# Performance work log

Measured on AMD Instinct MI355X. Metric: run time of the kernel, lower is better.

The kernel has to match this reference:

```python
import jax, jax.numpy as jnp
import numpy as np

B, S, E, D = 4, 2048, 1024, 64  # batch, seq, embed_size, low-rank d; dv = E

def setup_inputs() -> dict:
    key = jax.random.key(0)
    ks = jax.random.split(key, 10)
    sc_e = 1.0 / np.sqrt(E)
    sc_d = 1.0 / np.sqrt(D)
    return {
        "x": jax.random.normal(ks[0], (B, S, E), jnp.float32),
        "y": jax.random.normal(ks[1], (B, S, E), jnp.float32),
        "Wq": jax.random.uniform(ks[2], (D, E), jnp.float32, -sc_e, sc_e),
        "bq": jax.random.uniform(ks[3], (D,), jnp.float32, -sc_e, sc_e),
        "Wk": jax.random.uniform(ks[4], (D, E), jnp.float32, -sc_e, sc_e),
        "bk": jax.random.uniform(ks[5], (D,), jnp.float32, -sc_e, sc_e),
        "WvR": jax.random.uniform(ks[6], (D, E), jnp.float32, -sc_e, sc_e),
        "bvR": jax.random.uniform(ks[7], (D,), jnp.float32, -sc_e, sc_e),
        "WvL": jax.random.uniform(ks[8], (E, D), jnp.float32, -sc_d, sc_d),
        "bvL": jax.random.uniform(ks[9], (E,), jnp.float32, -sc_d, sc_d),
    }

def reference(x, y, Wq, bq, Wk, bk, WvR, bvR, WvL, bvL):
    d = Wq.shape[0]
    Q = jnp.einsum('bse,de->bsd', x, Wq) + bq            # [B,S,D]
    K = jnp.einsum('bse,de->bsd', y, Wk) + bk            # [B,S,D]
    scores = jnp.einsum('bqd,bkd->bqk', Q, K) / jnp.sqrt(jnp.float32(d))
    # NOTE: original softmaxes over dim=1, i.e. the QUERY axis (faithful quirk)
    attn = jax.nn.softmax(scores, axis=1)                # [B,Sq,Sk]
    V = jnp.einsum('bsd,vd->bsv', jnp.einsum('bse,de->bsd', y, WvR) + bvR, WvL) + bvL  # [B,S,E]
    return jnp.einsum('bqk,bkv->bqv', attn, V)           # [B,S,E]
```

## Files before the change

### kernel.cpp

```cpp
#include <hip/hip_runtime.h>
#include <hip/hip_bf16.h>

#define DEV static __device__ __forceinline__
#define AS1 __attribute__((address_space(1)))
#define AS3 __attribute__((address_space(3)))

typedef __attribute__((ext_vector_type(8))) short bf16x8;
typedef __attribute__((ext_vector_type(4))) short bf16x4;
typedef __attribute__((ext_vector_type(4))) float f32x4;

constexpr int NB = 4;
constexpr int SS = 2048;
constexpr int EE = 1024;
constexpr int DD = 64;
constexpr int MTOT = NB * SS;

#define QSCALE (0.125f * 1.44269504088896340736f)

DEV short f2bf(float f) {
    union { float f; unsigned u; } v; v.f = f;
    unsigned u = v.u;
    u += 0x7FFFu + ((u >> 16) & 1u);
    return (short)(u >> 16);
}
DEV float bf2f(short h) {
    union { unsigned u; float f; } v; v.u = ((unsigned)(unsigned short)h) << 16;
    return v.f;
}
DEV unsigned pk2(float a, float b) {
    unsigned r;
    asm("v_cvt_pk_bf16_f32 %0, %1, %2" : "=v"(r) : "v"(a), "v"(b));
    return r;
}

DEV f32x4 mfma16(bf16x8 a, bf16x8 b, f32x4 c) {
    return __builtin_amdgcn_mfma_f32_16x16x32_bf16(a, b, c, 0, 0, 0);
}

DEV float redmax16(float v) {
    v = fmaxf(v, __shfl_xor(v, 1)); v = fmaxf(v, __shfl_xor(v, 2));
    v = fmaxf(v, __shfl_xor(v, 4)); v = fmaxf(v, __shfl_xor(v, 8));
    return v;
}
DEV float redsum16(float v) {
    v += __shfl_xor(v, 1); v += __shfl_xor(v, 2);
    v += __shfl_xor(v, 4); v += __shfl_xor(v, 8);
    return v;
}


__global__ __launch_bounds__(256) void k_prep(
    const float* __restrict__ Wq, const float* __restrict__ Wk,
    const float* __restrict__ Wv, const float* __restrict__ WvL,
    const float* __restrict__ bvL,
    short* __restrict__ Wqb, short* __restrict__ Wkb, short* __restrict__ Wvb,
    short* __restrict__ Wcat2)
{
    int g = blockIdx.x * 256 + threadIdx.x;
    if (g < 24576) {
        int mat = g >> 13;
        int c = g & 8191;
        int lane = c & 63;
        int fn = (c >> 6) & 3;
        int it = (c >> 8) & 7;
        int kq4 = c >> 11;
        int r = lane & 15, half = lane >> 4;
        int row = fn * 16 + r;
        int col = kq4 * 256 + it * 32 + half * 4;
        const float* W = (mat == 0) ? Wq : ((mat == 1) ? Wk : Wv);
        short* O = (mat == 0) ? Wqb : ((mat == 1) ? Wkb : Wvb);
        float s = (mat == 0) ? QSCALE : 1.0f;
        const float* Wp = W + (size_t)row * EE + col;
        float4 u = *(const float4*)(Wp);
        float4 v = *(const float4*)(Wp + 16);
        bf16x8 o;
        unsigned* ou = (unsigned*)&o;
        ou[0] = pk2(u.x * s, u.y * s);
        ou[1] = pk2(u.z * s, u.w * s);
        ou[2] = pk2(v.x * s, v.y * s);
        ou[3] = pk2(v.z * s, v.w * s);
        *(bf16x8*)(O + (size_t)c * 8) = o;
    } else {
        int i2 = g - 24576;
        int lane = i2 & 63;
        int ks = (i2 >> 6) % 5;
        int vt = i2 / 320;
        int r = lane & 15, h = lane >> 4;
        int v = vt * 16 + r;
        bf16x8 o;
        #pragma unroll
        for (int j = 0; j < 8; ++j) {
            int c = ks * 16 + (h & 1) * 8 + j;
            float val = (c < 64) ? WvL[(size_t)v * DD + c] : ((c == 64) ? bvL[v] : 0.f);
            o[j] = f2bf(val);
        }
        *(bf16x8*)(Wcat2 + ((size_t)(vt * 5 + ks) * 64 + lane) * 8) = o;
    }
}

__global__ __launch_bounds__(256, 4) void k_proj(
    const float* __restrict__ x, const float* __restrict__ y,
    const short* __restrict__ Wqb, const short* __restrict__ Wkb,
    const short* __restrict__ Wvb,
    const float* __restrict__ bq, const float* __restrict__ bk,
    const float* __restrict__ bv,
    short* __restrict__ Qf, short* __restrict__ Kf, short* __restrict__ VF)
{
    const int tid = threadIdx.x, wave = tid >> 6, lane = tid & 63;
    const int r = lane & 15, half = lane >> 4;
    const int rb = blockIdx.x * 16;
    const bool isQ = (blockIdx.y == 0);
    const float* src = isQ ? x : y;
    const short* wA = isQ ? Wqb : Wkb;
    const int kq = wave * 256;

    __shared__ f32x4 red[4][8][64];

    f32x4 accA[4] = {}, accB[4] = {};
    const float* arow = src + (size_t)(rb + r) * EE + kq + half * 4;
    const short* wbase = wA + (size_t)wave * 16384 + lane * 8;
    const short* vbase = Wvb + (size_t)wave * 16384 + lane * 8;

    float4 af0[8], af1[8];
    #pragma unroll
    for (int it = 0; it < 8; ++it) {
        af0[it] = *(const float4*)(arow + it * 32);
        af1[it] = *(const float4*)(arow + it * 32 + 16);
    }

    #pragma unroll
    for (int it = 0; it < 8; ++it) {
        bf16x8 a;
        unsigned* au = (unsigned*)&a;
        au[0] = pk2(af0[it].x, af0[it].y);
        au[1] = pk2(af0[it].z, af0[it].w);
        au[2] = pk2(af1[it].x, af1[it].y);
        au[3] = pk2(af1[it].z, af1[it].w);
        #pragma unroll
        for (int n = 0; n < 4; ++n) {
            bf16x8 b = *(const bf16x8*)(wbase + (it * 4 + n) * 64 * 8);
            accA[n] = mfma16(a, b, accA[n]);
        }
        if (!isQ) {
            #pragma unroll
            for (int n = 0; n < 4; ++n) {
                bf16x8 b = *(const bf16x8*)(vbase + (it * 4 + n) * 64 * 8);
                accB[n] = mfma16(a, b, accB[n]);
            }
        }
    }

    #pragma unroll
    for (int n = 0; n < 4; ++n) red[wave][n][lane] = accA[n];
    if (!isQ) {
        #pragma unroll
        for (int n = 0; n < 4; ++n) red[wave][4 + n][lane] = accB[n];
    }
    __syncthreads();

    const int n = wave;
    const int col = n * 16 + r;
    f32x4 s = red[0][n][lane];
    #pragma unroll
    for (int w = 1; w < 4; ++w) s += red[w][n][lane];
    float biasA = isQ ? (bq[col] * QSCALE) : bk[col];
    f32x4 t = {};
    float biasB = 0.f;
    if (!isQ) {
        t = red[0][4 + n][lane];
        #pragma unroll
        for (int w = 1; w < 4; ++w) t += red[w][4 + n][lane];
        biasB = bv[col];
    }
    __syncthreads();
    float* tlA = (float*)&red[0][0][0];
    float* tlB = tlA + 16 * 68;
    #pragma unroll
    for (int ri = 0; ri < 4; ++ri)
        tlA[(half * 4 + ri) * 68 + col] = s[ri] + biasA;
    if (!isQ) {
        #pragma unroll
        for (int ri = 0; ri < 4; ++ri)
            tlB[(half * 4 + ri) * 68 + col] = t[ri] + biasB;
    }
    __syncthreads();
    if (tid < 128) {
        int h2 = tid >> 6, l2 = tid & 63, r2 = l2 & 15, hh = l2 >> 4;
        const float* base = tlA + r2 * 68 + h2 * 32 + hh * 8;
        bf16x8 o;
        unsigned* ou = (unsigned*)&o;
        #pragma unroll
        for (int jj = 0; jj < 4; ++jj)
            ou[jj] = pk2(base[2 * jj], base[2 * jj + 1]);
        short* dst = (isQ ? Qf : Kf) + ((size_t)blockIdx.x * 2 + h2) * 512 + l2 * 8;
        *(bf16x8*)dst = o;
    } else if (!isQ) {
        int idx = tid - 128;
        int nn = idx >> 5, sub = idx & 31;
        int r2 = sub & 15, su = sub >> 4;
        int hbase = (rb & 16) ? 2 : 0;
        int lane2 = ((hbase + su) << 4) | r2;
        const float* base = tlB + (size_t)su * 8 * 68 + nn * 16 + r2;
        bf16x8 o;
        unsigned* ou = (unsigned*)&o;
        #pragma unroll
        for (int jj = 0; jj < 4; ++jj)
            ou[jj] = pk2(base[(2 * jj) * 68], base[(2 * jj + 1) * 68]);
        int batch = rb >> 11;
        int cg2 = (rb & 2047) >> 5;
        *(bf16x8*)(VF + (((size_t)batch * 64 + cg2) * 4 + nn) * 512 + lane2 * 8) = o;
    }
}

__global__ __launch_bounds__(512) void k_stats(
    const short* __restrict__ Qf, const short* __restrict__ Kf,
    float* __restrict__ Ml, float* __restrict__ Rl)
{
    const int tid = threadIdx.x, wave = tid >> 6, lane = tid & 63;
    const int r = lane & 15, half = lane >> 4;
    const int batch = blockIdx.y;
    const int kb = blockIdx.x * 16;

    __shared__ float smax[8][16], ssum[8][16];

    const short* kfp = Kf + ((size_t)(batch * 128 + (kb >> 4)) * 2) * 512 + lane * 8;
    bf16x8 kf0 = *(const bf16x8*)kfp;
    bf16x8 kf1 = *(const bf16x8*)(kfp + 512);

    const int qt0 = batch * 128 + wave * 16;
    f32x4 s[16];
    #pragma unroll
    for (int t = 0; t < 16; ++t) {
        const short* qp = Qf + ((size_t)(qt0 + t) * 2) * 512 + lane * 8;
        bf16x8 a0 = *(const bf16x8*)qp;
        bf16x8 a1 = *(const bf16x8*)(qp + 512);
        f32x4 c = {};
        c = mfma16(kf0, a0, c);
        c = mfma16(kf1, a1, c);
        s[t] = c;
    }
    f32x4 m4 = s[0];
    #pragma unroll
    for (int t = 1; t < 16; ++t) {
        #pragma unroll
        for (int ri = 0; ri < 4; ++ri) m4[ri] = fmaxf(m4[ri], s[t][ri]);
    }
    #pragma unroll
    for (int ri = 0; ri < 4; ++ri) m4[ri] = redmax16(m4[ri]);
    if (r == 0) {
        #pragma unroll
        for (int ri = 0; ri < 4; ++ri) smax[wave][half * 4 + ri] = m4[ri];
    }
    __syncthreads();
    f32x4 M;
    #pragma unroll
    for (int ri = 0; ri < 4; ++ri) {
        float v = smax[0][half * 4 + ri];
        #pragma unroll
        for (int w = 1; w < 8; ++w) v = fmaxf(v, smax[w][half * 4 + ri]);
        M[ri] = v;
    }
    f32x4 l4 = {};
    #pragma unroll
    for (int t = 0; t < 16; ++t)
        #pragma unroll
        for (int ri = 0; ri < 4; ++ri) l4[ri] += exp2f(s[t][ri] - M[ri]);
    #pragma unroll
    for (int ri = 0; ri < 4; ++ri) l4[ri] = redsum16(l4[ri]);
    if (r == 0) {
        #pragma unroll
        for (int ri = 0; ri < 4; ++ri) ssum[wave][half * 4 + ri] = l4[ri];
    }
    __syncthreads();
    if (wave == 0 && r == 0) {
        f32x4 rl;
        #pragma unroll
        for (int ri = 0; ri < 4; ++ri) {
            float v = 0.f;
            #pragma unroll
            for (int w = 0; w < 8; ++w) v += ssum[w][half * 4 + ri];
            rl[ri] = 1.0f / v;
        }
        *(f32x4*)(Ml + (size_t)batch * SS + kb + half * 4) = M;
        *(f32x4*)(Rl + (size_t)batch * SS + kb + half * 4) = rl;
    }
}

__global__ __launch_bounds__(512) void k_pvfuse(
    const short* __restrict__ Qf, const short* __restrict__ Kf,
    const short* __restrict__ VF,
    const float* __restrict__ Ml, const float* __restrict__ Rl,
    short* __restrict__ Tcat2)
{
    const int tid = threadIdx.x, wave = tid >> 6, lane = tid & 63;
    const int r = lane & 15, half = lane >> 4;
    const int bid = blockIdx.x;
    const int qt = (bid & 7) * 64 + (bid >> 3);
    const int batch = qt >> 7;
    const int kbase = wave * 256;

    __shared__ short pl[8][16][40];
    __shared__ f32x4 red2[8][5][64];
    __shared__ float tl2[16][84];

    const short* qp = Qf + (size_t)qt * 2 * 512 + lane * 8;
    bf16x8 qf0 = *(const bf16x8*)qp;
    bf16x8 qf1 = *(const bf16x8*)(qp + 512);
    bf16x8 ones;
    #pragma unroll
    for (int j = 0; j < 8; ++j) ones[j] = (r == 0) ? (short)0x3F80 : (short)0;

    const float* mlb = Ml + (size_t)batch * SS;
    const float* rlb = Rl + (size_t)batch * SS;
    const short* kfb = Kf + (size_t)batch * 128 * 1024;
    const short* vfb = VF + (size_t)batch * 64 * 4 * 512;

    f32x4 acc[5] = {};

    #pragma unroll 2
    for (int st = 0; st < 8; ++st) {
        const int kt = kbase + st * 32;
        const short* kp = kfb + (size_t)(kt >> 4) * 1024 + lane * 8;
        bf16x8 k00 = *(const bf16x8*)kp;
        bf16x8 k01 = *(const bf16x8*)(kp + 512);
        bf16x8 k10 = *(const bf16x8*)(kp + 1024);
        bf16x8 k11 = *(const bf16x8*)(kp + 1536);
        f32x4 s0 = {}, s1 = {};
        s0 = mfma16(k00, qf0, s0); s0 = mfma16(k01, qf1, s0);
        s1 = mfma16(k10, qf0, s1); s1 = mfma16(k11, qf1, s1);
        f32x4 m0 = *(const f32x4*)(mlb + kt + half * 4);
        f32x4 r0 = *(const f32x4*)(rlb + kt + half * 4);
        f32x4 m1 = *(const f32x4*)(mlb + kt + 16 + half * 4);
        f32x4 r1 = *(const f32x4*)(rlb + kt + 16 + half * 4);
        f32x4 p0, p1;
        #pragma unroll
        for (int ri = 0; ri < 4; ++ri) {
            p0[ri] = exp2f(s0[ri] - m0[ri]) * r0[ri];
            p1[ri] = exp2f(s1[ri] - m1[ri]) * r1[ri];
        }
        uint2 u0, u1;
        u0.x = pk2(p0[0], p0[1]); u0.y = pk2(p0[2], p0[3]);
        u1.x = pk2(p1[0], p1[1]); u1.y = pk2(p1[2], p1[3]);
        *(uint2*)&pl[wave][r][4 * half] = u0;
        *(uint2*)&pl[wave][r][16 + 4 * half] = u1;
        bf16x8 af = *(const bf16x8*)&pl[wave][r][half * 8];
        #pragma unroll
        for (int nn = 0; nn < 4; ++nn) {
            bf16x8 vf = *(const bf16x8*)(vfb + ((size_t)(kt >> 5) * 4 + nn) * 512 + lane * 8);
            acc[nn] = mfma16(af, vf, acc[nn]);
        }
        acc[4] = mfma16(af, ones, acc[4]);
    }

    #pragma unroll
    for (int nn = 0; nn < 5; ++nn) red2[wave][nn][lane] = acc[nn];
    __syncthreads();
    if (wave < 5) {
        int nn = wave;
        f32x4 v = red2[0][nn][lane];
        #pragma unroll
        for (int w = 1; w < 8; ++w) v += red2[w][nn][lane];
        #pragma unroll
        for (int ri = 0; ri < 4; ++ri) tl2[half * 4 + ri][nn * 16 + r] = v[ri];
    }
    __syncthreads();
    if (tid < 320) {
        int ks = tid >> 6;
        int l2 = tid & 63;
        int r2 = l2 & 15, h2 = l2 >> 4;
        bf16x8 o;
        #pragma unroll
        for (int j = 0; j < 8; ++j) {
            float v = tl2[r2][ks * 16 + (h2 & 1) * 8 + j];
            short hi = f2bf(v);
            o[j] = (h2 < 2) ? hi : f2bf(v - bf2f(hi));
        }
        *(bf16x8*)(Tcat2 + (((size_t)qt * 5 + ks) * 64 + l2) * 8) = o;
    }
}

__global__ __launch_bounds__(256) void k_gemm2(
    const short* __restrict__ Tcat2, const short* __restrict__ Wcat2,
    float* __restrict__ out)
{
    const int tid = threadIdx.x, wave = tid >> 6, lane = tid & 63;
    const int r = lane & 15, half = lane >> 4;
    const int wm = wave >> 1, wn = wave & 1;
    const int bid = blockIdx.x;
    const int w = (bid & 7) * 64 + (bid >> 3);
    const int qB = (w >> 3) * 128;
    const int vB = (w & 7) * 128;
    const int tA0 = qB / 16 + wm * 4;
    const int vt0 = vB / 16 + wn * 4;

    f32x4 acc[4][4] = {};
    #pragma unroll
    for (int ks = 0; ks < 5; ++ks) {
        bf16x8 a[4], b[4];
        #pragma unroll
        for (int i = 0; i < 4; ++i) {
            a[i] = *(const bf16x8*)(Tcat2 + ((size_t)(tA0 + i) * 5 + ks) * 512 + lane * 8);
            b[i] = *(const bf16x8*)(Wcat2 + ((size_t)(vt0 + i) * 5 + ks) * 512 + lane * 8);
        }
        #pragma unroll
        for (int mi = 0; mi < 4; ++mi)
            #pragma unroll
            for (int ni = 0; ni < 4; ++ni)
                acc[mi][ni] = mfma16(a[mi], b[ni], acc[mi][ni]);
    }

    const int r4 = half * 4;
    #pragma unroll
    for (int mi = 0; mi < 4; ++mi)
        #pragma unroll
        for (int ni = 0; ni < 4; ++ni)
            #pragma unroll
            for (int ri = 0; ri < 4; ++ri)
                out[(size_t)(qB + wm * 64 + mi * 16 + r4 + ri) * EE + vB + wn * 64 + ni * 16 + r] = acc[mi][ni][ri];
}

extern "C" void kernel_launch(void* const* d_in, const int* in_sizes, int n_in,
                              void* d_out, int out_size, void* d_ws, size_t ws_size,
                              hipStream_t stream) {
    (void)in_sizes; (void)n_in; (void)out_size; (void)ws_size;
    const float* x   = (const float*)d_in[0];
    const float* y   = (const float*)d_in[1];
    const float* Wq  = (const float*)d_in[2];
    const float* bq  = (const float*)d_in[3];
    const float* Wk  = (const float*)d_in[4];
    const float* bk  = (const float*)d_in[5];
    const float* WvR = (const float*)d_in[6];
    const float* bvR = (const float*)d_in[7];
    const float* WvL = (const float*)d_in[8];
    const float* bvL = (const float*)d_in[9];
    float* out = (float*)d_out;

    short* Qf    = (short*)d_ws;
    short* Kf    = Qf    + (size_t)MTOT * DD;
    short* VF    = Kf    + (size_t)MTOT * DD;
    short* Tcat2 = VF    + (size_t)MTOT * DD;
    short* Wqb   = Tcat2 + (size_t)(MTOT / 16) * 5 * 512;
    short* Wkb   = Wqb   + (size_t)DD * EE;
    short* Wvb   = Wkb   + (size_t)DD * EE;
    short* Wcat2 = Wvb   + (size_t)DD * EE;
    float* Ml    = (float*)(Wcat2 + (size_t)64 * 5 * 512);
    float* Rl    = Ml + MTOT;

    k_prep<<<dim3(176), 256, 0, stream>>>(Wq, Wk, WvR, WvL, bvL, Wqb, Wkb, Wvb, Wcat2);
    k_proj<<<dim3(MTOT / 16, 2), 256, 0, stream>>>(x, y, Wqb, Wkb, Wvb, bq, bk, bvR, Qf, Kf, VF);
    k_stats<<<dim3(SS / 16, NB), 512, 0, stream>>>(Qf, Kf, Ml, Rl);
    k_pvfuse<<<dim3(512), 512, 0, stream>>>(Qf, Kf, VF, Ml, Rl, Tcat2);
    k_gemm2<<<dim3(512), 256, 0, stream>>>(Tcat2, Wcat2, out);
}
```

Before: 67.71 us.

## Tile projection over 64 rows with LDS double-buffered weights; add setprio around MFMAs

The projection kernel now handles 64 rows per 512-thread block and stages the bf16 weight slices into LDS through double-buffered global_load_lds, so four row-groups share each weight fetch instead of every 16-row block reading the weights from global memory. The K dimension is split into two halves with a single LDS reduction, and the Q/K/V output packing is adapted to the larger tile. The attention kernel also raises wave priority around its MFMA sequences. The trade-offs are a barrier per K-step, fewer blocks in the grid, and more LDS use per block.

```diff
diff --git a/kernel.cpp b/kernel.cpp
--- a/kernel.cpp
+++ b/kernel.cpp
@@ -98,7 +98,17 @@
     }
 }
 
-__global__ __launch_bounds__(256, 4) void k_proj(
+#define PJ_STAGE(buf, s) {                                                     \
+    const short* s1_ = wA + ((size_t)(khT * 16 + (s)) * 2048) + t2 * 8;        \
+    __builtin_amdgcn_global_load_lds((const AS1 void*)s1_,                     \
+        (AS3 void*)(&wst[buf][wldsb]), 16, 0, 0);                              \
+    if (!isQ) {                                                                \
+        const short* s2_ = Wvb + ((size_t)(khT * 16 + (s)) * 2048) + t2 * 8;   \
+        __builtin_amdgcn_global_load_lds((const AS1 void*)s2_,                 \
+            (AS3 void*)(&wst[buf][wldsb + 2048]), 16, 0, 0);                   \
+    } }
+
+__global__ __launch_bounds__(512) void k_proj(
     const float* __restrict__ x, const float* __restrict__ y,
     const short* __restrict__ Wqb, const short* __restrict__ Wkb,
     const short* __restrict__ Wvb,
@@ -108,107 +118,133 @@
 {
     const int tid = threadIdx.x, wave = tid >> 6, lane = tid & 63;
     const int r = lane & 15, half = lane >> 4;
-    const int rb = blockIdx.x * 16;
+    const int rb = blockIdx.x * 64;
     const bool isQ = (blockIdx.y == 0);
     const float* src = isQ ? x : y;
     const short* wA = isQ ? Wqb : Wkb;
-    const int kq = wave * 256;
-
-    __shared__ f32x4 red[4][8][64];
+    const int rg = wave & 3, kh = wave >> 2;
+
+    const int khT = wave >> 2;
+    const int t2 = tid & 255;
+    const int wldsb = khT * 4096 + (wave & 3) * 512;
+
+    __shared__ __align__(16) short wst[2][8192];
+    __shared__ float tl[64][68];
 
     f32x4 accA[4] = {}, accB[4] = {};
-    const float* arow = src + (size_t)(rb + r) * EE + kq + half * 4;
-    const short* wbase = wA + (size_t)wave * 16384 + lane * 8;
-    const short* vbase = Wvb + (size_t)wave * 16384 + lane * 8;
-
-    float4 af0[8], af1[8];
-    #pragma unroll
-    for (int it = 0; it < 8; ++it) {
-        af0[it] = *(const float4*)(arow + it * 32);
-        af1[it] = *(const float4*)(arow + it * 32 + 16);
-    }
-
-    #pragma unroll
-    for (int it = 0; it < 8; ++it) {
+    const float* arow = src + (size_t)(rb + rg * 16 + r) * EE + kh * 512 + half * 4;
+
+    PJ_STAGE(0, 0)
+    __syncthreads();
+
+    float4 a0c = *(const float4*)(arow);
+    float4 a1c = *(const float4*)(arow + 16);
+    float4 a0n, a1n;
+
+    int buf = 0;
+    #pragma unroll 4
+    for (int s = 0; s < 16; ++s) {
+        if (s + 1 < 16) {
+            PJ_STAGE(buf ^ 1, s + 1)
+            a0n = *(const float4*)(arow + (s + 1) * 32);
+            a1n = *(const float4*)(arow + (s + 1) * 32 + 16);
+        }
         bf16x8 a;
         unsigned* au = (unsigned*)&a;
-        au[0] = pk2(af0[it].x, af0[it].y);
-        au[1] = pk2(af0[it].z, af0[it].w);
-        au[2] = pk2(af1[it].x, af1[it].y);
-        au[3] = pk2(af1[it].z, af1[it].w);
+        au[0] = pk2(a0c.x, a0c.y);
+        au[1] = pk2(a0c.z, a0c.w);
+        au[2] = pk2(a1c.x, a1c.y);
+        au[3] = pk2(a1c.z, a1c.w);
+        const short* wsl = &wst[buf][kh * 4096];
         #pragma unroll
         for (int n = 0; n < 4; ++n) {
-            bf16x8 b = *(const bf16x8*)(wbase + (it * 4 + n) * 64 * 8);
-            accA[n] = mfma16(a, b, accA[n]);
+            bf16x8 bw = *(const bf16x8*)(wsl + n * 512 + lane * 8);
+            accA[n] = mfma16(a, bw, accA[n]);
         }
         if (!isQ) {
             #pragma unroll
             for (int n = 0; n < 4; ++n) {
-                bf16x8 b = *(const bf16x8*)(vbase + (it * 4 + n) * 64 * 8);
-                accB[n] = mfma16(a, b, accB[n]);
+                bf16x8 bv_ = *(const bf16x8*)(wsl + 2048 + n * 512 + lane * 8);
+                accB[n] = mfma16(a, bv_, accB[n]);
             }
         }
-    }
-
-    #pragma unroll
-    for (int n = 0; n < 4; ++n) red[wave][n][lane] = accA[n];
-    if (!isQ) {
-        #pragma unroll
-        for (int n = 0; n < 4; ++n) red[wave][4 + n][lane] = accB[n];
-    }
-    __syncthreads();
-
-    const int n = wave;
-    const int col = n * 16 + r;
-    f32x4 s = red[0][n][lane];
-    #pragma unroll
-    for (int w = 1; w < 4; ++w) s += red[w][n][lane];
-    float biasA = isQ ? (bq[col] * QSCALE) : bk[col];
-    f32x4 t = {};
-    float biasB = 0.f;
-    if (!isQ) {
-        t = red[0][4 + n][lane];
-        #pragma unroll
-        for (int w = 1; w < 4; ++w) t += red[w][4 + n][lane];
-        biasB = bv[col];
-    }
-    __syncthreads();
-    float* tlA = (float*)&red[0][0][0];
-    float* tlB = tlA + 16 * 68;
-    #pragma unroll
-    for (int ri = 0; ri < 4; ++ri)
-        tlA[(half * 4 + ri) * 68 + col] = s[ri] + biasA;
-    if (!isQ) {
-        #pragma unroll
-        for (int ri = 0; ri < 4; ++ri)
-            tlB[(half * 4 + ri) * 68 + col] = t[ri] + biasB;
-    }
-    __syncthreads();
-    if (tid < 128) {
-        int h2 = tid >> 6, l2 = tid & 63, r2 = l2 & 15, hh = l2 >> 4;
-        const float* base = tlA + r2 * 68 + h2 * 32 + hh * 8;
+        a0c = a0n; a1c = a1n;
+        __syncthreads();
+        buf ^= 1;
+    }
+
+    f32x4* red = (f32x4*)&wst[0][0];
+    if (kh == 1) {
+        #pragma unroll
+        for (int n = 0; n < 4; ++n) red[((rg * 2 + 0) * 4 + n) * 64 + lane] = accA[n];
+        if (!isQ) {
+            #pragma unroll
+            for (int n = 0; n < 4; ++n) red[((rg * 2 + 1) * 4 + n) * 64 + lane] = accB[n];
+        }
+    }
+    __syncthreads();
+    if (kh == 0) {
+        #pragma unroll
+        for (int n = 0; n < 4; ++n) accA[n] += red[((rg * 2 + 0) * 4 + n) * 64 + lane];
+        if (!isQ) {
+            #pragma unroll
+            for (int n = 0; n < 4; ++n) accB[n] += red[((rg * 2 + 1) * 4 + n) * 64 + lane];
+        }
+    }
+    __syncthreads();
+
+    if (kh == 0) {
+        #pragma unroll
+        for (int n = 0; n < 4; ++n) {
+            int col = n * 16 + r;
+            float bias = isQ ? (bq[col] * QSCALE) : bk[col];
+            #pragma unroll
+            for (int ri = 0; ri < 4; ++ri)
+                tl[rg * 16 + half * 4 + ri][col] = accA[n][ri] + bias;
+        }
+    }
+    __syncthreads();
+    {
+        int tt = tid >> 7;
+        int h2 = (tid >> 6) & 1;
+        int l2 = tid & 63, r2 = l2 & 15, hh = l2 >> 4;
+        const float* base = &tl[tt * 16 + r2][h2 * 32 + hh * 8];
         bf16x8 o;
         unsigned* ou = (unsigned*)&o;
         #pragma unroll
         for (int jj = 0; jj < 4; ++jj)
             ou[jj] = pk2(base[2 * jj], base[2 * jj + 1]);
-        short* dst = (isQ ? Qf : Kf) + ((size_t)blockIdx.x * 2 + h2) * 512 + l2 * 8;
+        short* dst = (isQ ? Qf : Kf) + ((size_t)(rb / 16 + tt) * 2 + h2) * 512 + l2 * 8;
         *(bf16x8*)dst = o;
-    } else if (!isQ) {
-        int idx = tid - 128;
-        int nn = idx >> 5, sub = idx & 31;
-        int r2 = sub & 15, su = sub >> 4;
-        int hbase = (rb & 16) ? 2 : 0;
-        int lane2 = ((hbase + su) << 4) | r2;
-        const float* base = tlB + (size_t)su * 8 * 68 + nn * 16 + r2;
-        bf16x8 o;
-        unsigned* ou = (unsigned*)&o;
-        #pragma unroll
-        for (int jj = 0; jj < 4; ++jj)
-            ou[jj] = pk2(base[(2 * jj) * 68], base[(2 * jj + 1) * 68]);
-        int batch = rb >> 11;
-        int cg2 = (rb & 2047) >> 5;
-        *(bf16x8*)(VF + (((size_t)batch * 64 + cg2) * 4 + nn) * 512 + lane2 * 8) = o;
+    }
+
+    if (!isQ) {
+        __syncthreads();
+        if (kh == 0) {
+            #pragma unroll
+            for (int n = 0; n < 4; ++n) {
+                int col = n * 16 + r;
+                float bias = bv[col];
+                #pragma unroll
+                for (int ri = 0; ri < 4; ++ri)
+                    tl[rg * 16 + half * 4 + ri][col] = accB[n][ri] + bias;
+            }
+        }
+        __syncthreads();
+        {
+            int cgl = tid >> 8;
+            int nn = (tid >> 6) & 3;
+            int l2 = tid & 63, r2 = l2 & 15, h2q = l2 >> 4;
+            bf16x8 o;
+            unsigned* ou = (unsigned*)&o;
+            #pragma unroll
+            for (int jj = 0; jj < 4; ++jj)
+                ou[jj] = pk2(tl[cgl * 32 + h2q * 8 + 2 * jj][nn * 16 + r2],
+                             tl[cgl * 32 + h2q * 8 + 2 * jj + 1][nn * 16 + r2]);
+            int batch = rb >> 11;
+            int cg2 = ((rb & 2047) >> 5) + cgl;
+            *(bf16x8*)(VF + (((size_t)batch * 64 + cg2) * 4 + nn) * 512 + l2 * 8) = o;
+        }
     }
 }
 
@@ -326,8 +362,10 @@
         bf16x8 k10 = *(const bf16x8*)(kp + 1024);
         bf16x8 k11 = *(const bf16x8*)(kp + 1536);
         f32x4 s0 = {}, s1 = {};
+        __builtin_amdgcn_s_setprio(1);
         s0 = mfma16(k00, qf0, s0); s0 = mfma16(k01, qf1, s0);
         s1 = mfma16(k10, qf0, s1); s1 = mfma16(k11, qf1, s1);
+        __builtin_amdgcn_s_setprio(0);
         f32x4 m0 = *(const f32x4*)(mlb + kt + half * 4);
         f32x4 r0 = *(const f32x4*)(rlb + kt + half * 4);
         f32x4 m1 = *(const f32x4*)(mlb + kt + 16 + half * 4);
@@ -344,12 +382,14 @@
         *(uint2*)&pl[wave][r][4 * half] = u0;
         *(uint2*)&pl[wave][r][16 + 4 * half] = u1;
         bf16x8 af = *(const bf16x8*)&pl[wave][r][half * 8];
+        __builtin_amdgcn_s_setprio(1);
         #pragma unroll
         for (int nn = 0; nn < 4; ++nn) {
             bf16x8 vf = *(const bf16x8*)(vfb + ((size_t)(kt >> 5) * 4 + nn) * 512 + lane * 8);
             acc[nn] = mfma16(af, vf, acc[nn]);
         }
         acc[4] = mfma16(af, ones, acc[4]);
+        __builtin_amdgcn_s_setprio(0);
     }
 
     #pragma unroll
@@ -447,7 +487,7 @@
     float* Rl    = Ml + MTOT;
 
     k_prep<<<dim3(176), 256, 0, stream>>>(Wq, Wk, WvR, WvL, bvL, Wqb, Wkb, Wvb, Wcat2);
-    k_proj<<<dim3(MTOT / 16, 2), 256, 0, stream>>>(x, y, Wqb, Wkb, Wvb, bq, bk, bvR, Qf, Kf, VF);
+    k_proj<<<dim3(MTOT / 64, 2), 512, 0, stream>>>(x, y, Wqb, Wkb, Wvb, bq, bk, bvR, Qf, Kf, VF);
     k_stats<<<dim3(SS / 16, NB), 512, 0, stream>>>(Qf, Kf, Ml, Rl);
     k_pvfuse<<<dim3(512), 512, 0, stream>>>(Qf, Kf, VF, Ml, Rl, Tcat2);
     k_gemm2<<<dim3(512), 256, 0, stream>>>(Tcat2, Wcat2, out);
```

Result: faster. 65.04 us (-4.0%).
